# Optimization experiments

Measured on AMD Instinct MI355X. Metric: run time of the kernel, lower is better.

Reference implementation:

```python
import jax, jax.numpy as jnp
import numpy as np

_EPS = 1e-3            # distance_eps
_COEFF = 0.42 * 0.2 * 332.0
_LEN_NH = 1.015
_CUT_E = -0.5
_CUT_D = 3.6
_CUT_GAP = 3


def collect_neighbors(x, edge_idx):
    # x: (B, N, D), edge_idx: (B, N, K) -> (B, N, K, D)
    return jax.vmap(lambda xb, eb: xb[eb])(x, edge_idx)


def normed_vec(v):
    return v / jnp.sqrt(jnp.sum(v * v, axis=-1, keepdims=True) + _EPS)


def setup_inputs() -> dict:
    key = jax.random.key(0)
    k1, k2, k3 = jax.random.split(key, 3)
    B, N, K = 4, 16384, 64
    X = jax.random.normal(k1, (B, N, 4, 3), dtype=jnp.float32) * 3.0
    C = jnp.sort(jax.random.randint(k2, (B, N), 1, 9), axis=-1).astype(jnp.int64)
    edge_idx = jax.random.randint(k3, (B, N, K), 0, N).astype(jnp.int64)
    mask_ij = jnp.ones((B, N, K), dtype=jnp.float32)
    return {"X": X, "C": C, "edge_idx": edge_idx, "mask_ij": mask_ij}


def reference(X, C, edge_idx, mask_ij):
    B, N = X.shape[0], X.shape[1]
    # gather neighbor backbone atoms: (B, N, K, 4, 3)
    X_j = collect_neighbors(X.reshape(B, N, 12), edge_idx).reshape(B, N, -1, 4, 3)

    # previous residue (replicate-pad at front)
    X_prev = jnp.concatenate([X[:, :1], X[:, :-1]], axis=1)
    C_prev_i = X_prev[:, :, 2, :]          # carbonyl C of residue i-1
    N_i = X[:, :, 0, :]
    Ca_i = X[:, :, 1, :]

    # virtual hydrogen placement
    u_NH = normed_vec(normed_vec(N_i - C_prev_i) + normed_vec(N_i - Ca_i))
    H_i = N_i + _LEN_NH * u_NH             # (B, N, 3)

    Nq = N_i[:, :, None, :]                # (B, N, 1, 3)
    Hq = H_i[:, :, None, :]
    O_j = X_j[:, :, :, 3, :]               # (B, N, K, 3)
    C_j = X_j[:, :, :, 2, :]

    invD = lambda a, b: 1.0 / jnp.sqrt(jnp.sum((a - b) ** 2, axis=-1) + _EPS)
    U_ij = _COEFF * (invD(Nq, O_j) - invD(Nq, C_j) + invD(Hq, C_j) - invD(Hq, O_j))

    D_NO = jnp.sqrt(jnp.sum((Nq - O_j) ** 2, axis=-1) + _EPS)
    mask_cut_D = (D_NO < _CUT_D).astype(jnp.float32)

    # locality mask: same chain and |i-j| < cutoff_gap (note jx == edge_idx)
    Cn = collect_neighbors(C[..., None], edge_idx)[..., 0]          # (B, N, K)
    dij = jnp.abs(edge_idx - jnp.arange(N)[None, :, None])
    mask_local = ((dij < _CUT_GAP) & (C[:, :, None] == Cn)).astype(jnp.float32)
    mask_nonlocal = 1.0 - mask_local

    # NOTE: in the source, F.pad(C,[1,0])[:,1:] reproduces C itself, so
    # mask_i reduces to (C > 0); we replicate that math faithfully.
    C_prev = jnp.concatenate([jnp.zeros_like(C[:, :1]), C], axis=1)[:, 1:]
    mask_i = ((C > 0) & (C == C_prev)).astype(jnp.float32)
    mask_internal = mask_i[..., None] * (Cn > 0).astype(jnp.float32)

    mask_hb_ij = mask_ij * mask_nonlocal * mask_cut_D * mask_internal
    hbonds = mask_hb_ij * (U_ij < _CUT_E).astype(jnp.float32)
    return hbonds, mask_hb_ij, H_i[:, :, None, :]
```

## Files before the change

### kernel.cpp

```cpp
#include <hip/hip_runtime.h>

static __device__ __forceinline__ float sq3(float x, float y, float z) {
    return __fadd_rn(__fadd_rn(__fmul_rn(x, x), __fmul_rn(y, y)), __fmul_rn(z, z));
}

__global__ __launch_bounds__(256) void setup_kernel(
    const float* __restrict__ X,
    const int*   __restrict__ C,
    float*  __restrict__ outH,
    float4* __restrict__ T,
    int N, int rows)
{
    const float EPS   = 0.001f;
    const float LENNH = 1.015f;

    int row = blockIdx.x * blockDim.x + threadIdx.x;
    if (row >= rows) return;
    int i = row & (N - 1);

    const float* xi = X + (size_t)row * 12;
    float4 a4  = *(const float4*)xi;
    float2 a2  = *(const float2*)(xi + 4);
    float2 c01 = *(const float2*)(xi + 6);
    float4 co  = *(const float4*)(xi + 8);
    float nx = a4.x, ny = a4.y, nz = a4.z;
    float cax = a4.w, cay = a2.x, caz = a2.y;

    if (T) {
        T[2 * (size_t)row]     = make_float4(c01.x, c01.y, co.x, co.y);
        T[2 * (size_t)row + 1] = make_float4(co.z, co.w, __int_as_float(C[row]), 0.0f);
    }

    int prow = (i == 0) ? row : row - 1;
    const float* xp = X + (size_t)prow * 12;
    float2 p2 = *(const float2*)(xp + 6);
    float px = p2.x, py = p2.y, pz = xp[8];

    float ax = __fsub_rn(nx, px), ay = __fsub_rn(ny, py), az = __fsub_rn(nz, pz);
    float s1 = __fsqrt_rn(__fadd_rn(sq3(ax, ay, az), EPS));
    ax = __fdiv_rn(ax, s1); ay = __fdiv_rn(ay, s1); az = __fdiv_rn(az, s1);
    float bx = __fsub_rn(nx, cax), by = __fsub_rn(ny, cay), bz = __fsub_rn(nz, caz);
    float s2 = __fsqrt_rn(__fadd_rn(sq3(bx, by, bz), EPS));
    bx = __fdiv_rn(bx, s2); by = __fdiv_rn(by, s2); bz = __fdiv_rn(bz, s2);
    float ux = __fadd_rn(ax, bx), uy = __fadd_rn(ay, by), uz = __fadd_rn(az, bz);
    float s3 = __fsqrt_rn(__fadd_rn(sq3(ux, uy, uz), EPS));
    ux = __fdiv_rn(ux, s3); uy = __fdiv_rn(uy, s3); uz = __fdiv_rn(uz, s3);

    float* ho = outH + (size_t)row * 3;
    ho[0] = __fadd_rn(nx, __fmul_rn(LENNH, ux));
    ho[1] = __fadd_rn(ny, __fmul_rn(LENNH, uy));
    ho[2] = __fadd_rn(nz, __fmul_rn(LENNH, uz));
}

static __device__ __forceinline__ void edge_math(
    float nx, float ny, float nz, float hx, float hy, float hz,
    int Ci, int i, int j, float mij, float4 t0, float4 t1,
    float& hb, float& mhb)
{
    const float EPS   = 0.001f;
    const float COEFF = (float)(0.42 * 0.2 * 332.0);

    float cjx = t0.x, cjy = t0.y, cjz = t0.z;
    float ojx = t0.w, ojy = t1.x, ojz = t1.y;
    int   Cn  = __float_as_int(t1.z);

    float dx = __fsub_rn(nx, ojx), dy = __fsub_rn(ny, ojy), dz = __fsub_rn(nz, ojz);
    float dno = __fsqrt_rn(__fadd_rn(sq3(dx, dy, dz), EPS));
    float iNO = __fdiv_rn(1.0f, dno);
    dx = __fsub_rn(nx, cjx); dy = __fsub_rn(ny, cjy); dz = __fsub_rn(nz, cjz);
    float iNC = __fdiv_rn(1.0f, __fsqrt_rn(__fadd_rn(sq3(dx, dy, dz), EPS)));
    dx = __fsub_rn(hx, cjx); dy = __fsub_rn(hy, cjy); dz = __fsub_rn(hz, cjz);
    float iHC = __fdiv_rn(1.0f, __fsqrt_rn(__fadd_rn(sq3(dx, dy, dz), EPS)));
    dx = __fsub_rn(hx, ojx); dy = __fsub_rn(hy, ojy); dz = __fsub_rn(hz, ojz);
    float iHO = __fdiv_rn(1.0f, __fsqrt_rn(__fadd_rn(sq3(dx, dy, dz), EPS)));

    float U = __fmul_rn(COEFF, __fsub_rn(__fadd_rn(__fsub_rn(iNO, iNC), iHC), iHO));

    int dij = j - i; if (dij < 0) dij = -dij;
    float m_local    = ((dij < 3) && (Ci == Cn)) ? 1.0f : 0.0f;
    float m_nonlocal = __fsub_rn(1.0f, m_local);
    float m_cutD     = (dno < 3.6f) ? 1.0f : 0.0f;
    float m_i        = (Ci > 0) ? 1.0f : 0.0f;
    float m_int      = __fmul_rn(m_i, (Cn > 0) ? 1.0f : 0.0f);

    mhb = __fmul_rn(__fmul_rn(__fmul_rn(mij, m_nonlocal), m_cutD), m_int);
    hb  = __fmul_rn(mhb, (U < -0.5f) ? 1.0f : 0.0f);
}

__global__ __launch_bounds__(256) void edge_kernel4(
    const int*   __restrict__ C,
    const int*   __restrict__ E,
    const float* __restrict__ M,
    const float* __restrict__ H,
    const float* __restrict__ X,
    const float4* __restrict__ T,
    float* __restrict__ outHB,
    float* __restrict__ outMK,
    int N, int rows)
{
    int tid = blockIdx.x * blockDim.x + threadIdx.x;
    int row = tid >> 4;
    if (row >= rows) return;
    int k0 = (tid & 15) << 2;
    int i = row & (N - 1);
    int b = row >> 14;

    const float* xi = X + (size_t)row * 12;
    float nx = xi[0], ny = xi[1], nz = xi[2];
    const float* hi = H + (size_t)row * 3;
    float hx = hi[0], hy = hi[1], hz = hi[2];
    int Ci = C[row];

    size_t eoff = (size_t)row * 64 + (size_t)k0;
    int4   j4 = *(const int4*)(E + eoff);
    float4 m4 = *(const float4*)(M + eoff);

    const float4* Tb = T + ((size_t)b << 15);
    float4 t0a = Tb[2 * (size_t)j4.x],     t1a = Tb[2 * (size_t)j4.x + 1];
    float4 t0b = Tb[2 * (size_t)j4.y],     t1b = Tb[2 * (size_t)j4.y + 1];
    float4 t0c = Tb[2 * (size_t)j4.z],     t1c = Tb[2 * (size_t)j4.z + 1];
    float4 t0d = Tb[2 * (size_t)j4.w],     t1d = Tb[2 * (size_t)j4.w + 1];

    float4 hbv, mkv;
    edge_math(nx, ny, nz, hx, hy, hz, Ci, i, j4.x, m4.x, t0a, t1a, hbv.x, mkv.x);
    edge_math(nx, ny, nz, hx, hy, hz, Ci, i, j4.y, m4.y, t0b, t1b, hbv.y, mkv.y);
    edge_math(nx, ny, nz, hx, hy, hz, Ci, i, j4.z, m4.z, t0c, t1c, hbv.z, mkv.z);
    edge_math(nx, ny, nz, hx, hy, hz, Ci, i, j4.w, m4.w, t0d, t1d, hbv.w, mkv.w);

    *(float4*)(outHB + eoff) = hbv;
    *(float4*)(outMK + eoff) = mkv;
}

__global__ __launch_bounds__(256) void edge_kernel_noT(
    const float* __restrict__ X,
    const int*   __restrict__ C,
    const int*   __restrict__ E,
    const float* __restrict__ M,
    const float* __restrict__ H,
    float* __restrict__ outHB,
    float* __restrict__ outMK,
    int N, int rows)
{
    int tid = blockIdx.x * blockDim.x + threadIdx.x;
    int row = tid >> 6;
    if (row >= rows) return;
    int k = tid & 63;
    int i = row & (N - 1);
    int b = row >> 14;

    int urow = __builtin_amdgcn_readfirstlane(row);
    const float* xi = X + (size_t)urow * 12;
    float nx = xi[0], ny = xi[1], nz = xi[2];
    const float* hi = H + (size_t)urow * 3;
    float hx = hi[0], hy = hi[1], hz = hi[2];
    int Ci = C[urow];

    size_t eoff = (size_t)row * 64 + (size_t)k;
    int j = E[eoff];
    float mij = M[eoff];

    const float* xj = X + ((size_t)b * (size_t)N + (size_t)j) * 12;
    float2 cj01 = *(const float2*)(xj + 6);
    float4 v4   = *(const float4*)(xj + 8);
    int Cn = C[(size_t)b * (size_t)N + (size_t)j];

    float4 t0 = make_float4(cj01.x, cj01.y, v4.x, v4.y);
    float4 t1 = make_float4(v4.z, v4.w, __int_as_float(Cn), 0.0f);
    float hb, mhb;
    edge_math(nx, ny, nz, hx, hy, hz, Ci, i, j, mij, t0, t1, hb, mhb);

    outHB[eoff] = hb;
    outMK[eoff] = mhb;
}

extern "C" void kernel_launch(void* const* d_in, const int* in_sizes, int n_in,
                              void* d_out, int out_size, void* d_ws, size_t ws_size,
                              hipStream_t stream) {
    const float* X = (const float*)d_in[0];
    const int*   C = (const int*)d_in[1];
    const int*   E = (const int*)d_in[2];
    const float* M = (const float*)d_in[3];

    int rows = in_sizes[1];
    int BNK  = in_sizes[2];
    const int N = 16384;

    float* out   = (float*)d_out;
    float* outHB = out;
    float* outMK = out + (size_t)BNK;
    float* outH  = out + 2 * (size_t)BNK;

    size_t tbytes = (size_t)rows * 32;
    bool useT = (ws_size >= tbytes) && (d_ws != nullptr);
    float4* T = useT ? (float4*)d_ws : nullptr;

    {
        int block = 256;
        int grid  = (rows + block - 1) / block;
        hipLaunchKernelGGL(setup_kernel, dim3(grid), dim3(block), 0, stream,
                           X, C, outH, T, N, rows);
    }
    if (useT) {
        int total = rows * 16;
        int block = 256;
        int grid  = (total + block - 1) / block;
        hipLaunchKernelGGL(edge_kernel4, dim3(grid), dim3(block), 0, stream,
                           C, E, M, outH, X, T, outHB, outMK, N, rows);
    } else {
        int total = rows * 64;
        int block = 256;
        int grid  = (total + block - 1) / block;
        hipLaunchKernelGGL(edge_kernel_noT, dim3(grid), dim3(block), 0, stream,
                           X, C, E, M, outH, outHB, outMK, N, rows);
    }
}
```

Before: 36.31 us.

## Use one wavefront per row with lane-pair split gathers and shuffles

Replaces the 16-threads-per-row, 4-edges-per-thread edge kernel with a one-wavefront-per-row kernel. Each lane pair cooperatively gathers the two float4 halves of a neighbor's table entry and exchanges them with cross-lane shuffles, so each lane computes two edges. The aim is to spread random gathers across more lanes and get more memory-level parallelism, and to load row-uniform values through a scalar path. In exchange it launches four times as many threads, adds shuffle traffic, replaces vector float4 stores with scalar stores, and each thread computes the full math for both edges.

```diff
diff --git a/kernel.cpp b/kernel.cpp
--- a/kernel.cpp
+++ b/kernel.cpp
@@ -87,7 +87,7 @@
     hb  = __fmul_rn(mhb, (U < -0.5f) ? 1.0f : 0.0f);
 }
 
-__global__ __launch_bounds__(256) void edge_kernel4(
+__global__ __launch_bounds__(256) void edge_kernel_pair(
     const int*   __restrict__ C,
     const int*   __restrict__ E,
     const float* __restrict__ M,
@@ -98,37 +98,60 @@
     float* __restrict__ outMK,
     int N, int rows)
 {
-    int tid = blockIdx.x * blockDim.x + threadIdx.x;
-    int row = tid >> 4;
+    int gtid = blockIdx.x * blockDim.x + threadIdx.x;
+    int row  = gtid >> 6;
     if (row >= rows) return;
-    int k0 = (tid & 15) << 2;
+    int lane = threadIdx.x & 63;
     int i = row & (N - 1);
     int b = row >> 14;
 
-    const float* xi = X + (size_t)row * 12;
+    int urow = __builtin_amdgcn_readfirstlane(row);
+    const float* xi = X + (size_t)urow * 12;
     float nx = xi[0], ny = xi[1], nz = xi[2];
-    const float* hi = H + (size_t)row * 3;
+    const float* hi = H + (size_t)urow * 3;
     float hx = hi[0], hy = hi[1], hz = hi[2];
-    int Ci = C[row];
-
-    size_t eoff = (size_t)row * 64 + (size_t)k0;
-    int4   j4 = *(const int4*)(E + eoff);
-    float4 m4 = *(const float4*)(M + eoff);
+    int Ci = C[urow];
+
+    size_t base = (size_t)row * 64;
+    int   jall = E[base + lane];
+    float mall = M[base + lane];
 
     const float4* Tb = T + ((size_t)b << 15);
-    float4 t0a = Tb[2 * (size_t)j4.x],     t1a = Tb[2 * (size_t)j4.x + 1];
-    float4 t0b = Tb[2 * (size_t)j4.y],     t1b = Tb[2 * (size_t)j4.y + 1];
-    float4 t0c = Tb[2 * (size_t)j4.z],     t1c = Tb[2 * (size_t)j4.z + 1];
-    float4 t0d = Tb[2 * (size_t)j4.w],     t1d = Tb[2 * (size_t)j4.w + 1];
-
-    float4 hbv, mkv;
-    edge_math(nx, ny, nz, hx, hy, hz, Ci, i, j4.x, m4.x, t0a, t1a, hbv.x, mkv.x);
-    edge_math(nx, ny, nz, hx, hy, hz, Ci, i, j4.y, m4.y, t0b, t1b, hbv.y, mkv.y);
-    edge_math(nx, ny, nz, hx, hy, hz, Ci, i, j4.z, m4.z, t0c, t1c, hbv.z, mkv.z);
-    edge_math(nx, ny, nz, hx, hy, hz, Ci, i, j4.w, m4.w, t0d, t1d, hbv.w, mkv.w);
-
-    *(float4*)(outHB + eoff) = hbv;
-    *(float4*)(outMK + eoff) = mkv;
+    int half = lane & 1;
+    int e0 = lane >> 1;
+    int e1 = 32 + e0;
+
+    int   j0 = __shfl(jall, e0, 64);
+    int   j1 = __shfl(jall, e1, 64);
+    float m0 = __shfl(mall, e0, 64);
+    float m1 = __shfl(mall, e1, 64);
+
+    float4 mine0 = Tb[2 * (size_t)j0 + half];
+    float4 mine1 = Tb[2 * (size_t)j1 + half];
+
+    float4 oth0, oth1;
+    oth0.x = __shfl_xor(mine0.x, 1, 64);
+    oth0.y = __shfl_xor(mine0.y, 1, 64);
+    oth0.z = __shfl_xor(mine0.z, 1, 64);
+    oth0.w = __shfl_xor(mine0.w, 1, 64);
+    oth1.x = __shfl_xor(mine1.x, 1, 64);
+    oth1.y = __shfl_xor(mine1.y, 1, 64);
+    oth1.z = __shfl_xor(mine1.z, 1, 64);
+    oth1.w = __shfl_xor(mine1.w, 1, 64);
+
+    float4 t0a = half ? oth0 : mine0;
+    float4 t1a = half ? mine0 : oth0;
+    float4 t0b = half ? oth1 : mine1;
+    float4 t1b = half ? mine1 : oth1;
+
+    float hb0, mk0, hb1, mk1;
+    edge_math(nx, ny, nz, hx, hy, hz, Ci, i, j0, m0, t0a, t1a, hb0, mk0);
+    edge_math(nx, ny, nz, hx, hy, hz, Ci, i, j1, m1, t0b, t1b, hb1, mk1);
+
+    outHB[base + e0] = hb0;
+    outMK[base + e0] = mk0;
+    outHB[base + e1] = hb1;
+    outMK[base + e1] = mk1;
 }
 
 __global__ __launch_bounds__(256) void edge_kernel_noT(
@@ -201,10 +224,10 @@
                            X, C, outH, T, N, rows);
     }
     if (useT) {
-        int total = rows * 16;
+        int total = rows * 64;
         int block = 256;
         int grid  = (total + block - 1) / block;
-        hipLaunchKernelGGL(edge_kernel4, dim3(grid), dim3(block), 0, stream,
+        hipLaunchKernelGGL(edge_kernel_pair, dim3(grid), dim3(block), 0, stream,
                            C, E, M, outH, X, T, outHB, outMK, N, rows);
     } else {
         int total = rows * 64;
```

Measured after the change: 40.57 us. +11.7%, slower.

## Restructure edge kernel to per-wave row loop with lane-pair split gathers

Applied to the files above, without the earlier changes.

Replaces the 4-edges-per-thread edge kernel with a persistent-style kernel. Each wave handles several rows and processes two rows per iteration for more memory parallelism. Each lane pair splits the two 16-byte halves of a neighbor's 32-byte table record, loads one half each, and exchanges the halves with xor-1 shuffles, so each thread issues one float4 gather per edge instead of two. The aim is better coalescing of the gathers and fewer redundant per-row loads. In exchange it adds shuffle traffic, scalar stores instead of float4 stores, and a grid capped near 8192 waves, which may reduce parallelism.

```diff
diff --git a/kernel.cpp b/kernel.cpp
--- a/kernel.cpp
+++ b/kernel.cpp
@@ -87,7 +87,16 @@
     hb  = __fmul_rn(mhb, (U < -0.5f) ? 1.0f : 0.0f);
 }
 
-__global__ __launch_bounds__(256) void edge_kernel4(
+static __device__ __forceinline__ float4 swapx1(float4 v) {
+    float4 r;
+    r.x = __shfl_xor(v.x, 1, 64);
+    r.y = __shfl_xor(v.y, 1, 64);
+    r.z = __shfl_xor(v.z, 1, 64);
+    r.w = __shfl_xor(v.w, 1, 64);
+    return r;
+}
+
+__global__ __launch_bounds__(256) void edge_kernel_ilp(
     const int*   __restrict__ C,
     const int*   __restrict__ E,
     const float* __restrict__ M,
@@ -96,39 +105,70 @@
     const float4* __restrict__ T,
     float* __restrict__ outHB,
     float* __restrict__ outMK,
-    int N, int rows)
-{
-    int tid = blockIdx.x * blockDim.x + threadIdx.x;
-    int row = tid >> 4;
-    if (row >= rows) return;
-    int k0 = (tid & 15) << 2;
-    int i = row & (N - 1);
-    int b = row >> 14;
-
-    const float* xi = X + (size_t)row * 12;
-    float nx = xi[0], ny = xi[1], nz = xi[2];
-    const float* hi = H + (size_t)row * 3;
-    float hx = hi[0], hy = hi[1], hz = hi[2];
-    int Ci = C[row];
-
-    size_t eoff = (size_t)row * 64 + (size_t)k0;
-    int4   j4 = *(const int4*)(E + eoff);
-    float4 m4 = *(const float4*)(M + eoff);
-
-    const float4* Tb = T + ((size_t)b << 15);
-    float4 t0a = Tb[2 * (size_t)j4.x],     t1a = Tb[2 * (size_t)j4.x + 1];
-    float4 t0b = Tb[2 * (size_t)j4.y],     t1b = Tb[2 * (size_t)j4.y + 1];
-    float4 t0c = Tb[2 * (size_t)j4.z],     t1c = Tb[2 * (size_t)j4.z + 1];
-    float4 t0d = Tb[2 * (size_t)j4.w],     t1d = Tb[2 * (size_t)j4.w + 1];
-
-    float4 hbv, mkv;
-    edge_math(nx, ny, nz, hx, hy, hz, Ci, i, j4.x, m4.x, t0a, t1a, hbv.x, mkv.x);
-    edge_math(nx, ny, nz, hx, hy, hz, Ci, i, j4.y, m4.y, t0b, t1b, hbv.y, mkv.y);
-    edge_math(nx, ny, nz, hx, hy, hz, Ci, i, j4.z, m4.z, t0c, t1c, hbv.z, mkv.z);
-    edge_math(nx, ny, nz, hx, hy, hz, Ci, i, j4.w, m4.w, t0d, t1d, hbv.w, mkv.w);
-
-    *(float4*)(outHB + eoff) = hbv;
-    *(float4*)(outMK + eoff) = mkv;
+    int N, int rows, int rpw)
+{
+    int gtid = blockIdx.x * blockDim.x + threadIdx.x;
+    int wave = __builtin_amdgcn_readfirstlane(gtid >> 6);
+    int lane = threadIdx.x & 63;
+    int e    = lane >> 1;
+    int half = lane & 1;
+    int eM   = (half << 5) | e;
+
+    int base_row = wave * rpw;
+    if (base_row >= rows) return;
+
+    for (int t = 0; t < rpw; t += 2) {
+        int rowA = base_row + t;
+        if (rowA >= rows) break;
+        int rowB = rowA + 1;
+        int iA = rowA & (N - 1), iB = rowB & (N - 1);
+        const float4* TbA = T + ((size_t)(rowA >> 14) << 15);
+        const float4* TbB = T + ((size_t)(rowB >> 14) << 15);
+
+        size_t bA = (size_t)rowA << 6;
+        size_t bB = (size_t)rowB << 6;
+
+        int jA0 = E[bA + e];
+        int jA1 = E[bA + 32 + e];
+        int jB0 = E[bB + e];
+        int jB1 = E[bB + 32 + e];
+        float mMA = M[bA + eM];
+        float mMB = M[bB + eM];
+
+        float4 vA0 = TbA[2 * (size_t)jA0 + half];
+        float4 vA1 = TbA[2 * (size_t)jA1 + (half ^ 1)];
+        float4 vB0 = TbB[2 * (size_t)jB0 + half];
+        float4 vB1 = TbB[2 * (size_t)jB1 + (half ^ 1)];
+
+        const float* xiA = X + (size_t)rowA * 12;
+        const float* hiA = H + (size_t)rowA * 3;
+        const float* xiB = X + (size_t)rowB * 12;
+        const float* hiB = H + (size_t)rowB * 3;
+        float nxA = xiA[0], nyA = xiA[1], nzA = xiA[2];
+        float hxA = hiA[0], hyA = hiA[1], hzA = hiA[2];
+        float nxB = xiB[0], nyB = xiB[1], nzB = xiB[2];
+        float hxB = hiB[0], hyB = hiB[1], hzB = hiB[2];
+        int CiA = C[rowA], CiB = C[rowB];
+
+        float4 wA0 = swapx1(vA0), wA1 = swapx1(vA1);
+        float4 wB0 = swapx1(vB0), wB1 = swapx1(vB1);
+
+        float4 t0A = half ? vA1 : vA0;
+        float4 t1A = half ? wA1 : wA0;
+        float4 t0B = half ? vB1 : vB0;
+        float4 t1B = half ? wB1 : wB0;
+        int jMA = half ? jA1 : jA0;
+        int jMB = half ? jB1 : jB0;
+
+        float hbA, mkA, hbB, mkB;
+        edge_math(nxA, nyA, nzA, hxA, hyA, hzA, CiA, iA, jMA, mMA, t0A, t1A, hbA, mkA);
+        edge_math(nxB, nyB, nzB, hxB, hyB, hzB, CiB, iB, jMB, mMB, t0B, t1B, hbB, mkB);
+
+        outHB[bA + eM] = hbA;
+        outMK[bA + eM] = mkA;
+        outHB[bB + eM] = hbB;
+        outMK[bB + eM] = mkB;
+    }
 }
 
 __global__ __launch_bounds__(256) void edge_kernel_noT(
@@ -201,11 +241,16 @@
                            X, C, outH, T, N, rows);
     }
     if (useT) {
-        int total = rows * 16;
+        int target_waves = 8192;
+        int rpw = (rows + target_waves - 1) / target_waves;
+        if (rpw & 1) rpw++;
+        if (rpw < 2) rpw = 2;
+        int waves = (rows + rpw - 1) / rpw;
+        int total = waves * 64;
         int block = 256;
         int grid  = (total + block - 1) / block;
-        hipLaunchKernelGGL(edge_kernel4, dim3(grid), dim3(block), 0, stream,
-                           C, E, M, outH, X, T, outHB, outMK, N, rows);
+        hipLaunchKernelGGL(edge_kernel_ilp, dim3(grid), dim3(block), 0, stream,
+                           C, E, M, outH, X, T, outHB, outMK, N, rows, rpw);
     } else {
         int total = rows * 64;
         int block = 256;
```

Measured after the change: 38.39 us. 1.06x slower.
